# Kernel optimization log

Hardware: AMD Instinct MI355X
Metric: run time of the kernel (lower is better)

Reference implementation:

```python
import jax, jax.numpy as jnp
import numpy as np

S = 7
BB = 2          # boxes per cell
C = 20          # classes
L_COORD = 5.0
L_NOOBJ = 0.5
L_OBJ = 1.0
L_CLASS = 1.0
BATCH = 8192


def setup_inputs() -> dict:
    key = jax.random.key(0)
    k1, k2, k3, k4 = jax.random.split(key, 4)
    pred = jax.random.normal(k1, (BATCH, S, S, BB * 5 + C), dtype=jnp.float32)
    cls = jax.random.uniform(k2, (BATCH, S, S, C), dtype=jnp.float32)
    # obj conf must be exactly 1.0 where an object exists (obj_mask test is ==1)
    conf = (jax.random.uniform(k3, (BATCH, S, S, 1)) < 0.3).astype(jnp.float32)
    box = jax.random.uniform(k4, (BATCH, S, S, 4), dtype=jnp.float32)  # cx,cy,w,h in [0,1)
    target = jnp.concatenate([cls, conf, box], axis=-1)
    return {"pred": pred, "target": target}


def _iou(a, b):
    # a: (..., BB, 4) cx,cy,w,h ; b: (..., 1, 4)  -> iou (..., BB)
    ax1, ay1 = a[..., 0] - a[..., 2] / 2, a[..., 1] - a[..., 3] / 2
    ax2, ay2 = a[..., 0] + a[..., 2] / 2, a[..., 1] + a[..., 3] / 2
    bx1, by1 = b[..., 0] - b[..., 2] / 2, b[..., 1] - b[..., 3] / 2
    bx2, by2 = b[..., 0] + b[..., 2] / 2, b[..., 1] + b[..., 3] / 2
    iw = jnp.clip(jnp.minimum(ax2, bx2) - jnp.maximum(ax1, bx1), 0.0)
    ih = jnp.clip(jnp.minimum(ay2, by2) - jnp.maximum(ay1, by1), 0.0)
    inter = iw * ih
    union = jnp.abs(a[..., 2] * a[..., 3]) + jnp.abs(b[..., 2] * b[..., 3]) - inter
    return inter / (union + 1e-6)


def reference(pred, target):
    # pred: (N,S,S,B*5+C), target: (N,S,S,5+C)
    objf = (target[..., C] == 1.0).astype(pred.dtype)        # (N,S,S)
    noobjf = 1.0 - objf
    pred_boxes = pred[..., C:].reshape(-1, S, S, BB, 5)       # (N,S,S,B,5) [conf,cx,cy,w,h]
    tb = target[..., C:]                                      # (N,S,S,5)

    ious = _iou(pred_boxes[..., 1:], tb[..., None, 1:])       # (N,S,S,B)
    best = jnp.argmax(ious, axis=-1)                          # responsible box index
    iou_best = jnp.max(ious, axis=-1)                         # (N,S,S)
    pb = jnp.take_along_axis(pred_boxes, best[..., None, None], axis=3)[..., 0, :]  # (N,S,S,5)

    center = jnp.sum((tb[..., 1:3] - pb[..., 1:3]) ** 2, axis=-1)
    # pred wh: pow(2).sqrt().sqrt() == sqrt(|wh|)
    wh = jnp.sum((jnp.sqrt(tb[..., 3:]) - jnp.sqrt(jnp.abs(pb[..., 3:]))) ** 2, axis=-1)
    conf_sq = (tb[..., 0] - pb[..., 0]) ** 2
    cls_sq = jnp.sum((pred[..., :C] - target[..., :C]) ** 2, axis=-1)

    loss = jnp.sum(
        objf * (L_COORD * (center + wh) + L_OBJ * conf_sq + L_CLASS * cls_sq)
        + noobjf * L_NOOBJ * conf_sq
    )
    avg_iou = jnp.sum(iou_best * objf) / jnp.maximum(jnp.sum(objf), 1.0)
    return loss, avg_iou
```

## Files before the change

kernel.cpp:

```cpp
#include <hip/hip_runtime.h>
#include <stdint.h>

#define S 7
#define BB 2
#define CLS 20
#define NCELLS (8192 * S * S)
#define CPB 64
#define THREADS 64
#define NBLK (NCELLS / CPB)
#define PRED_F 30
#define TGT_F 25

#define ASYNC_CP16(gsrc, ldst)                                                  \
    __builtin_amdgcn_global_load_lds(                                           \
        (const __attribute__((address_space(1))) void*)(gsrc),                  \
        (__attribute__((address_space(3))) void*)(ldst), 16, 0, 0)

__device__ __forceinline__ float iou_fn(float ax, float ay, float aw, float ah,
                                        float bx, float by, float bw, float bh) {
    float ax1 = ax - aw * 0.5f, ay1 = ay - ah * 0.5f;
    float ax2 = ax + aw * 0.5f, ay2 = ay + ah * 0.5f;
    float bx1 = bx - bw * 0.5f, by1 = by - bh * 0.5f;
    float bx2 = bx + bw * 0.5f, by2 = by + bh * 0.5f;
    float iw = fmaxf(fminf(ax2, bx2) - fmaxf(ax1, bx1), 0.0f);
    float ih = fmaxf(fminf(ay2, by2) - fmaxf(ay1, by1), 0.0f);
    float inter = iw * ih;
    float uni = fabsf(aw * ah) + fabsf(bw * bh) - inter;
    return inter / (uni + 1e-6f);
}

__global__ __launch_bounds__(THREADS) void yolo_main(const float* __restrict__ pred,
                                                     const float* __restrict__ tgt,
                                                     float4* __restrict__ part) {
    __shared__ float lp[CPB * PRED_F];
    __shared__ float lt[CPB * TGT_F];

    const int b = blockIdx.x;
    const int t = threadIdx.x;

    const float* gp = pred + (size_t)b * (CPB * PRED_F) + t * 4;
    #pragma unroll
    for (int i = 0; i < 7; ++i) {
        ASYNC_CP16(gp + i * 256, lp + i * 256);
    }
    if (t < 32) {
        ASYNC_CP16(gp + 7 * 256, lp + 7 * 256);
    }
    const float* gt = tgt + (size_t)b * (CPB * TGT_F) + t * 4;
    #pragma unroll
    for (int i = 0; i < 6; ++i) {
        ASYNC_CP16(gt + i * 256, lt + i * 256);
    }
    if (t < 16) {
        ASYNC_CP16(gt + 6 * 256, lt + 6 * 256);
    }
    __syncthreads();

    const float* pp = lp + t * PRED_F;
    const float* tp = lt + t * TGT_F;

    float tconf = tp[CLS + 0];
    float tx = tp[CLS + 1], ty = tp[CLS + 2], tw = tp[CLS + 3], th = tp[CLS + 4];

    float iou0 = iou_fn(pp[CLS + 1], pp[CLS + 2], pp[CLS + 3], pp[CLS + 4], tx, ty, tw, th);
    float iou1 = iou_fn(pp[CLS + 6], pp[CLS + 7], pp[CLS + 8], pp[CLS + 9], tx, ty, tw, th);
    int sel = (iou1 > iou0) ? 1 : 0;
    float iou_best = fmaxf(iou0, iou1);

    const float* pb = pp + CLS + sel * 5;
    float dx = tx - pb[1], dy = ty - pb[2];
    float center = dx * dx + dy * dy;
    float dw = sqrtf(tw) - sqrtf(fabsf(pb[3]));
    float dh = sqrtf(th) - sqrtf(fabsf(pb[4]));
    float wh = dw * dw + dh * dh;
    float dc = tconf - pb[0];
    float conf_sq = dc * dc;

    float cls_sq = 0.0f;
    #pragma unroll
    for (int k = 0; k < CLS; ++k) {
        float d = pp[k] - tp[k];
        cls_sq += d * d;
    }

    float objf = (tconf == 1.0f) ? 1.0f : 0.0f;
    float loss = objf * (5.0f * (center + wh) + conf_sq + cls_sq)
               + (1.0f - objf) * 0.5f * conf_sq;
    float iou_o = objf * iou_best;

    #pragma unroll
    for (int off = 32; off > 0; off >>= 1) {
        loss  += __shfl_down(loss,  off, 64);
        iou_o += __shfl_down(iou_o, off, 64);
        objf  += __shfl_down(objf,  off, 64);
    }
    if (t == 0) {
        part[b] = make_float4(loss, iou_o, objf, 0.0f);
    }
}

__global__ __launch_bounds__(1024) void yolo_fin(const float4* __restrict__ part,
                                                 float* __restrict__ out) {
    __shared__ float red[3][1024 / 64];
    float l = 0.f, i = 0.f, o = 0.f;
    for (int k = threadIdx.x; k < NBLK; k += 1024) {
        float4 v = part[k];
        l += v.x;
        i += v.y;
        o += v.z;
    }
    #pragma unroll
    for (int off = 32; off > 0; off >>= 1) {
        l += __shfl_down(l, off, 64);
        i += __shfl_down(i, off, 64);
        o += __shfl_down(o, off, 64);
    }
    const int wave = threadIdx.x >> 6, lane = threadIdx.x & 63;
    if (lane == 0) {
        red[0][wave] = l;
        red[1][wave] = i;
        red[2][wave] = o;
    }
    __syncthreads();
    if (threadIdx.x == 0) {
        float L = 0.f, I = 0.f, O = 0.f;
        #pragma unroll
        for (int w = 0; w < 1024 / 64; ++w) {
            L += red[0][w];
            I += red[1][w];
            O += red[2][w];
        }
        out[0] = L;
        out[1] = I / fmaxf(O, 1.0f);
    }
}

extern "C" void kernel_launch(void* const* d_in, const int* in_sizes, int n_in,
                              void* d_out, int out_size, void* d_ws, size_t ws_size,
                              hipStream_t stream) {
    const float* pred = (const float*)d_in[0];
    const float* tgt  = (const float*)d_in[1];
    float* out = (float*)d_out;
    float4* part = (float4*)d_ws;

    yolo_main<<<NBLK, THREADS, 0, stream>>>(pred, tgt, part);
    yolo_fin<<<1, 1024, 0, stream>>>(part, out);
}
```

Before: 105.3 us.

## Use persistent grid with double-buffered async LDS prefetch per wave

The main kernel becomes a persistent grid of 1280 single-wave blocks. Each block loops over 64-cell chunks with a stride of the grid size and double-buffers the global-to-LDS async copies, using explicit vmcnt and lgkmcnt waits so the next chunk's load overlaps the current chunk's compute. Per-thread partials are accumulated across chunks, which cuts the number of partials and lets the final reduction kernel shrink to 256 threads. The cost is fewer resident waves for hiding latency, and correctness now depends on hand-set waitcnt encodings matching the number of load instructions issued per chunk.

```diff
diff --git a/kernel.cpp b/kernel.cpp
--- a/kernel.cpp
+++ b/kernel.cpp
@@ -4,10 +4,10 @@
 #define S 7
 #define BB 2
 #define CLS 20
-#define NCELLS (8192 * S * S)
+#define NCHUNK (8192 * S * S / 64)
 #define CPB 64
 #define THREADS 64
-#define NBLK (NCELLS / CPB)
+#define GRID 1280
 #define PRED_F 30
 #define TGT_F 25
 
@@ -15,6 +15,10 @@
     __builtin_amdgcn_global_load_lds(                                           \
         (const __attribute__((address_space(1))) void*)(gsrc),                  \
         (__attribute__((address_space(3))) void*)(ldst), 16, 0, 0)
+
+#define WAIT_VM15()  __builtin_amdgcn_s_waitcnt(0x0F7F)
+#define WAIT_VM0()   __builtin_amdgcn_s_waitcnt(0x0F70)
+#define WAIT_LGKM0() __builtin_amdgcn_s_waitcnt(0xC07F)
 
 __device__ __forceinline__ float iou_fn(float ax, float ay, float aw, float ah,
                                         float bx, float by, float bw, float bh) {
@@ -29,81 +33,94 @@
     return inter / (uni + 1e-6f);
 }
 
+__device__ __forceinline__ void prefetch_chunk(const float* __restrict__ pred,
+                                               const float* __restrict__ tgt,
+                                               int c, float* lpb, float* ltb, int t) {
+    const float* gp = pred + (size_t)c * (CPB * PRED_F) + t * 4;
+    #pragma unroll
+    for (int i = 0; i < 7; ++i) ASYNC_CP16(gp + i * 256, lpb + i * 256);
+    if (t < 32) ASYNC_CP16(gp + 7 * 256, lpb + 7 * 256);
+    const float* gt = tgt + (size_t)c * (CPB * TGT_F) + t * 4;
+    #pragma unroll
+    for (int i = 0; i < 6; ++i) ASYNC_CP16(gt + i * 256, ltb + i * 256);
+    if (t < 16) ASYNC_CP16(gt + 6 * 256, ltb + 6 * 256);
+}
+
 __global__ __launch_bounds__(THREADS) void yolo_main(const float* __restrict__ pred,
                                                      const float* __restrict__ tgt,
                                                      float4* __restrict__ part) {
-    __shared__ float lp[CPB * PRED_F];
-    __shared__ float lt[CPB * TGT_F];
+    __shared__ float lp[2][CPB * PRED_F];
+    __shared__ float lt[2][CPB * TGT_F];
 
     const int b = blockIdx.x;
     const int t = threadIdx.x;
+    const int nch = (NCHUNK - b + GRID - 1) / GRID;
 
-    const float* gp = pred + (size_t)b * (CPB * PRED_F) + t * 4;
-    #pragma unroll
-    for (int i = 0; i < 7; ++i) {
-        ASYNC_CP16(gp + i * 256, lp + i * 256);
+    prefetch_chunk(pred, tgt, b, lp[0], lt[0], t);
+    if (nch > 1) prefetch_chunk(pred, tgt, b + GRID, lp[1], lt[1], t);
+
+    float accL = 0.f, accI = 0.f, accO = 0.f;
+
+    for (int k = 0; k < nch; ++k) {
+        if (k + 1 < nch) WAIT_VM15();
+        else             WAIT_VM0();
+
+        const float* pp = lp[k & 1] + t * PRED_F;
+        const float* tp = lt[k & 1] + t * TGT_F;
+
+        float tconf = tp[CLS + 0];
+        float tx = tp[CLS + 1], ty = tp[CLS + 2], tw = tp[CLS + 3], th = tp[CLS + 4];
+
+        float iou0 = iou_fn(pp[CLS + 1], pp[CLS + 2], pp[CLS + 3], pp[CLS + 4], tx, ty, tw, th);
+        float iou1 = iou_fn(pp[CLS + 6], pp[CLS + 7], pp[CLS + 8], pp[CLS + 9], tx, ty, tw, th);
+        int sel = (iou1 > iou0) ? 1 : 0;
+        float iou_best = fmaxf(iou0, iou1);
+
+        const float* pb = pp + CLS + sel * 5;
+        float dx = tx - pb[1], dy = ty - pb[2];
+        float center = dx * dx + dy * dy;
+        float dw = sqrtf(tw) - sqrtf(fabsf(pb[3]));
+        float dh = sqrtf(th) - sqrtf(fabsf(pb[4]));
+        float wh = dw * dw + dh * dh;
+        float dc = tconf - pb[0];
+        float conf_sq = dc * dc;
+
+        float cls_sq = 0.0f;
+        #pragma unroll
+        for (int j = 0; j < CLS; ++j) {
+            float d = pp[j] - tp[j];
+            cls_sq += d * d;
+        }
+
+        float objf = (tconf == 1.0f) ? 1.0f : 0.0f;
+        accL += objf * (5.0f * (center + wh) + conf_sq + cls_sq)
+              + (1.0f - objf) * 0.5f * conf_sq;
+        accI += objf * iou_best;
+        accO += objf;
+
+        int cnext = b + (k + 2) * GRID;
+        if (cnext < NCHUNK) {
+            WAIT_LGKM0();
+            prefetch_chunk(pred, tgt, cnext, lp[k & 1], lt[k & 1], t);
+        }
     }
-    if (t < 32) {
-        ASYNC_CP16(gp + 7 * 256, lp + 7 * 256);
-    }
-    const float* gt = tgt + (size_t)b * (CPB * TGT_F) + t * 4;
-    #pragma unroll
-    for (int i = 0; i < 6; ++i) {
-        ASYNC_CP16(gt + i * 256, lt + i * 256);
-    }
-    if (t < 16) {
-        ASYNC_CP16(gt + 6 * 256, lt + 6 * 256);
-    }
-    __syncthreads();
-
-    const float* pp = lp + t * PRED_F;
-    const float* tp = lt + t * TGT_F;
-
-    float tconf = tp[CLS + 0];
-    float tx = tp[CLS + 1], ty = tp[CLS + 2], tw = tp[CLS + 3], th = tp[CLS + 4];
-
-    float iou0 = iou_fn(pp[CLS + 1], pp[CLS + 2], pp[CLS + 3], pp[CLS + 4], tx, ty, tw, th);
-    float iou1 = iou_fn(pp[CLS + 6], pp[CLS + 7], pp[CLS + 8], pp[CLS + 9], tx, ty, tw, th);
-    int sel = (iou1 > iou0) ? 1 : 0;
-    float iou_best = fmaxf(iou0, iou1);
-
-    const float* pb = pp + CLS + sel * 5;
-    float dx = tx - pb[1], dy = ty - pb[2];
-    float center = dx * dx + dy * dy;
-    float dw = sqrtf(tw) - sqrtf(fabsf(pb[3]));
-    float dh = sqrtf(th) - sqrtf(fabsf(pb[4]));
-    float wh = dw * dw + dh * dh;
-    float dc = tconf - pb[0];
-    float conf_sq = dc * dc;
-
-    float cls_sq = 0.0f;
-    #pragma unroll
-    for (int k = 0; k < CLS; ++k) {
-        float d = pp[k] - tp[k];
-        cls_sq += d * d;
-    }
-
-    float objf = (tconf == 1.0f) ? 1.0f : 0.0f;
-    float loss = objf * (5.0f * (center + wh) + conf_sq + cls_sq)
-               + (1.0f - objf) * 0.5f * conf_sq;
-    float iou_o = objf * iou_best;
 
     #pragma unroll
     for (int off = 32; off > 0; off >>= 1) {
-        loss  += __shfl_down(loss,  off, 64);
-        iou_o += __shfl_down(iou_o, off, 64);
-        objf  += __shfl_down(objf,  off, 64);
+        accL += __shfl_down(accL, off, 64);
+        accI += __shfl_down(accI, off, 64);
+        accO += __shfl_down(accO, off, 64);
     }
     if (t == 0) {
-        part[b] = make_float4(loss, iou_o, objf, 0.0f);
+        part[b] = make_float4(accL, accI, accO, 0.0f);
     }
 }
 
-__global__ __launch_bounds__(1024) void yolo_fin(const float4* __restrict__ part,
-                                                 float* __restrict__ out) {
-    __shared__ float red[3][1024 / 64];
+__global__ __launch_bounds__(256) void yolo_fin(const float4* __restrict__ part,
+                                                float* __restrict__ out) {
+    __shared__ float red[3][256 / 64];
     float l = 0.f, i = 0.f, o = 0.f;
-    for (int k = threadIdx.x; k < NBLK; k += 1024) {
+    for (int k = threadIdx.x; k < GRID; k += 256) {
         float4 v = part[k];
         l += v.x;
         i += v.y;
@@ -125,7 +142,7 @@
     if (threadIdx.x == 0) {
         float L = 0.f, I = 0.f, O = 0.f;
         #pragma unroll
-        for (int w = 0; w < 1024 / 64; ++w) {
+        for (int w = 0; w < 4; ++w) {
             L += red[0][w];
             I += red[1][w];
             O += red[2][w];
@@ -143,6 +160,6 @@
     float* out = (float*)d_out;
     float4* part = (float4*)d_ws;
 
-    yolo_main<<<NBLK, THREADS, 0, stream>>>(pred, tgt, part);
-    yolo_fin<<<1, 1024, 0, stream>>>(part, out);
+    yolo_main<<<GRID, THREADS, 0, stream>>>(pred, tgt, part);
+    yolo_fin<<<1, 256, 0, stream>>>(part, out);
 }
```

Result: slower. 107.4 us (+2.0%).
